# Kernel optimization log

Hardware: AMD Instinct MI355X
Metric: run time of the kernel (lower is better)

The kernel has to match this reference:

```python
import jax, jax.numpy as jnp
import numpy as np

N = 10000      # nodes
ND = 64        # node_dim
H = 128        # hidden_dim
L = 4          # num_layers
K = 16         # knn k
TD = 16        # time_dim


def _time_embed(t, n):
    # sinusoidal embedding, matches _time_embed: freqs = exp(linspace(0,1,half)*-4)
    half = TD // 2
    freqs = jnp.exp(jnp.linspace(0.0, 1.0, half) * -4.0)            # [half]
    angles = t.reshape(1, 1) * freqs[None, :]                        # [1, half]
    emb = jnp.concatenate([jnp.sin(angles), jnp.cos(angles)], -1)    # [1, TD]
    return jnp.broadcast_to(emb, (n, TD))


def _knn_edges(pos, k):
    # full cdist + topk, mirroring _knn_graph (no_grad in torch)
    n = pos.shape[0]
    sq = jnp.sum(pos * pos, -1)
    d2 = sq[:, None] + sq[None, :] - 2.0 * (pos @ pos.T)             # [N, N]
    idxr = jnp.arange(n)
    d2 = d2.at[idxr, idxr].set(jnp.inf)
    _, nbr = jax.lax.top_k(-d2, k)                                   # [N, K] nearest
    src = jnp.repeat(idxr, k)
    dst = nbr.reshape(-1)
    return src, dst


def _egnn_layer(h, pos, src, dst, s, ew1, eb1, ew2, eb2, nw1, nb1, nw2, nb2, cw, cb):
    n = h.shape[0]
    diff = pos[dst] - pos[src]                                       # [E, 3]
    r2 = jnp.sum(diff * diff, -1, keepdims=True)                     # [E, 1]
    r = jnp.sqrt(r2 + 1e-8)
    dir_ij = diff / r
    e_in = jnp.concatenate([h[dst], h[src], r2], -1)                 # [E, 2H+1]
    m = jax.nn.silu(e_in @ ew1 + eb1)
    m = jax.nn.silu(m @ ew2 + eb2)                                   # [E, H]
    m = m * s[src][:, None]                                          # s-gate
    m_sum = jax.ops.segment_sum(m, dst, num_segments=n)              # [N, H]
    deg = jax.ops.segment_sum(jnp.ones((m.shape[0], 1), m.dtype), dst, num_segments=n)
    deg = jnp.maximum(deg, 1.0)
    m_sum = m_sum / deg
    hn = jax.nn.silu(jnp.concatenate([h, m_sum], -1) @ nw1 + nb1)
    h_new = hn @ nw2 + nb2                                           # [N, H]
    gamma = m @ cw + cb                                              # [E, 1]
    cu = jax.ops.segment_sum(gamma * dir_ij, dst, num_segments=n) / deg
    return h_new, pos + cu


def setup_inputs() -> dict:
    key = jax.random.key(0)
    ks = jax.random.split(key, 24)
    g = lambda k, shape: (jax.random.normal(k, shape, dtype=jnp.float32) * 0.05)
    z = lambda shape: jnp.zeros(shape, jnp.float32)
    return {
        'x': jax.random.normal(ks[0], (N, ND), jnp.float32),
        'pos': jax.random.normal(ks[1], (N, 3), jnp.float32) * 5.0,
        't': jax.random.uniform(ks[2], (1,), jnp.float32),
        's': jax.random.uniform(ks[3], (N,), jnp.float32),
        'proj_w': g(ks[4], (ND + 1 + TD, H)), 'proj_b': z((H,)),
        'edge_w1': g(ks[5], (L, 2 * H + 1, H)), 'edge_b1': z((L, H)),
        'edge_w2': g(ks[6], (L, H, H)), 'edge_b2': z((L, H)),
        'node_w1': g(ks[7], (L, 2 * H, H)), 'node_b1': z((L, H)),
        'node_w2': g(ks[8], (L, H, H)), 'node_b2': z((L, H)),
        'coord_w': g(ks[9], (L, H, 1)), 'coord_b': z((L, 1)),
        'ec_w': g(ks[10], (H, 3)), 'ec_b': z((3,)),
        'ef_w': g(ks[11], (H, ND)), 'ef_b': z((ND,)),
    }


def reference(x, pos, t, s, proj_w, proj_b, edge_w1, edge_b1, edge_w2, edge_b2,
              node_w1, node_b1, node_w2, node_b2, coord_w, coord_b,
              ec_w, ec_b, ef_w, ef_b):
    n = x.shape[0]
    src, dst = _knn_edges(jax.lax.stop_gradient(pos), K)  # graph build is no_grad
    temb = _time_embed(t[0], n)
    h = jnp.concatenate([x, s[:, None], temb], -1) @ proj_w + proj_b  # [N, H]
    p = pos
    for l in range(L):
        h, p = _egnn_layer(h, p, src, dst, s,
                           edge_w1[l], edge_b1[l], edge_w2[l], edge_b2[l],
                           node_w1[l], node_b1[l], node_w2[l], node_b2[l],
                           coord_w[l], coord_b[l])
    eps_c = h @ ec_w + ec_b                                           # [N, 3]
    eps_f = h @ ef_w + ef_b                                           # [N, ND]
    return jnp.concatenate([eps_c, eps_f, p], -1)                     # [N, 3+ND+3]
```

## Files before the change

### kernel.cpp

```cpp
#include <hip/hip_runtime.h>
#include <math.h>

#define N_NODES 10000
#define ND 64
#define H 128
#define LAYERS 4
#define KNN 16
#define TD 16
#define E_EDGES (N_NODES * KNN)
#define KC 1250
#define TILE_E 128

typedef __attribute__((ext_vector_type(8))) short short8;
typedef __attribute__((ext_vector_type(4))) float f32x4;

__device__ __forceinline__ float silu(float x) {
  return x * __builtin_amdgcn_rcpf(1.0f + __expf(-x));
}

__device__ __forceinline__ unsigned short f2bf(float f) {
  unsigned int u = __float_as_uint(f);
  u += 0x7fffu + ((u >> 16) & 1u);
  return (unsigned short)(u >> 16);
}
__device__ __forceinline__ float bf2f(unsigned short h) {
  return __uint_as_float(((unsigned int)h) << 16);
}

__global__ __launch_bounds__(256) void pos4_kernel(const float* __restrict__ pos,
                                                   float4* __restrict__ pos4,
                                                   float* __restrict__ p0,
                                                   int* __restrict__ degi) {
  int i = blockIdx.x * 256 + threadIdx.x;
  if (i >= N_NODES) return;
  float x = pos[i * 3 + 0], y = pos[i * 3 + 1], z = pos[i * 3 + 2];
  pos4[i] = make_float4(x, y, z, x * x + y * y + z * z);
  p0[i * 3 + 0] = x;
  p0[i * 3 + 1] = y;
  p0[i * 3 + 2] = z;
  degi[i] = 0;
}

__global__ __launch_bounds__(256) void wcvt_kernel(
    const float* __restrict__ ew2, const float* __restrict__ nw1,
    const float* __restrict__ nw2, const float* __restrict__ ew1,
    const float* __restrict__ pw, const float* __restrict__ ecw,
    const float* __restrict__ efw, unsigned short* __restrict__ w2T,
    unsigned short* __restrict__ nw1T, unsigned short* __restrict__ nw2T,
    unsigned short* __restrict__ ew1T, unsigned short* __restrict__ pwT,
    unsigned short* __restrict__ owT) {
  int i = blockIdx.x * 256 + threadIdx.x;
  if (i < 65536) {
    int l = i >> 14, rem = i & 16383, c = rem >> 7, o = rem & 127;
    w2T[l * 16384 + o * 128 + c] = f2bf(ew2[i]);
  } else if (i < 196608) {
    int j = i - 65536;
    int l = j >> 15, rem = j & 32767, c2 = rem >> 7, o = rem & 127;
    nw1T[l * 32768 + o * 256 + c2] = f2bf(nw1[j]);
  } else if (i < 262144) {
    int j = i - 196608;
    int l = j >> 14, rem = j & 16383, c = rem >> 7, o = rem & 127;
    nw2T[l * 16384 + o * 128 + c] = f2bf(nw2[j]);
  } else if (i < 393216) {
    int j = i - 262144;
    int l = j >> 15, rem = j & 32767, r = rem >> 7, o = rem & 127;
    int o2 = o + ((r >> 7) << 7);
    int c = r & 127;
    ew1T[l * 32768 + o2 * 128 + c] = f2bf(ew1[l * 257 * 128 + r * 128 + o]);
  } else if (i < 405504) {
    int j = i - 393216;
    int o = j / 96, c = j - o * 96;
    pwT[j] = (c < 81) ? f2bf(pw[c * 128 + o]) : 0;
  } else {
    int j = i - 405504;
    int o = j >> 7, c = j & 127;
    float v = 0.0f;
    if (o < 3) v = ecw[c * 3 + o];
    else if (o < 67) v = efw[c * 64 + (o - 3)];
    owT[j] = f2bf(v);
  }
}

#define DIST2(pp, d0, d1)                                                    \
  d0 = fmaf(ax0, (pp).x, fmaf(ay0, (pp).y, fmaf(az0, (pp).z, (pp).w)));      \
  d1 = fmaf(ax1, (pp).x, fmaf(ay1, (pp).y, fmaf(az1, (pp).z, (pp).w)));

#define PAIR(dv0, dv1, gbase)                                                \
  {                                                                          \
    unsigned long long m0 = __ballot((dv0) < th0);                           \
    unsigned long long m1 = __ballot((dv1) < th1);                           \
    if (m0 | m1) {                                                           \
      while (m0 | m1) {                                                      \
        if (m0) {                                                            \
          int sl = __ffsll((long long)m0) - 1;                               \
          m0 &= m0 - 1;                                                      \
          float db = __shfl((dv0), sl, 64);                                  \
          int gj = (gbase) + sl;                                             \
          float pv = __shfl_up(v0, 1, 64);                                   \
          int pid = __shfl_up(id0, 1, 64);                                   \
          bool stay = (v0 <= db);                                            \
          bool tk = (lane == 0) || (pv <= db);                               \
          v0 = stay ? v0 : (tk ? db : pv);                                   \
          id0 = stay ? id0 : (tk ? gj : pid);                                \
        }                                                                    \
        if (m1) {                                                            \
          int sl = __ffsll((long long)m1) - 1;                               \
          m1 &= m1 - 1;                                                      \
          float db = __shfl((dv1), sl, 64);                                  \
          int gj = (gbase) + sl;                                             \
          float pv = __shfl_up(v1, 1, 64);                                   \
          int pid = __shfl_up(id1, 1, 64);                                   \
          bool stay = (v1 <= db);                                            \
          bool tk = (lane == 0) || (pv <= db);                               \
          v1 = stay ? v1 : (tk ? db : pv);                                   \
          id1 = stay ? id1 : (tk ? gj : pid);                                \
        }                                                                    \
      }                                                                      \
      th0 = __shfl(v0, 16, 64);                                              \
      th1 = __shfl(v1, 16, 64);                                              \
    }                                                                        \
  }

__global__ __launch_bounds__(256) void knn_kernel(const float4* __restrict__ pos4,
                                                  int* __restrict__ nbr,
                                                  int* __restrict__ degi) {
  __shared__ float4 C[KC];
  int tid = threadIdx.x;
  int lane = tid & 63;
  int wid = tid >> 6;
  int qb = blockIdx.x * 8 + wid * 2;
  float4 q0 = pos4[qb];
  float4 q1 = pos4[qb + 1];
  float ax0 = -2.0f * q0.x, ay0 = -2.0f * q0.y, az0 = -2.0f * q0.z;
  float ax1 = -2.0f * q1.x, ay1 = -2.0f * q1.y, az1 = -2.0f * q1.z;
  float v0 = __builtin_inff(), v1 = __builtin_inff();
  int id0 = 0, id1 = 0;
  float th0 = __builtin_inff(), th1 = __builtin_inff();
  for (int base = 0; base < N_NODES; base += KC) {
    __syncthreads();
    for (int jj = tid; jj < KC; jj += 256) C[jj] = pos4[base + jj];
    __syncthreads();
    for (int j0 = 0; j0 < 1024; j0 += 256) {
      float4 pA = C[j0 + lane], pB = C[j0 + 64 + lane];
      float4 pC = C[j0 + 128 + lane], pD = C[j0 + 192 + lane];
      float dA0, dA1, dB0, dB1, dC0, dC1, dD0, dD1;
      DIST2(pA, dA0, dA1);
      DIST2(pB, dB0, dB1);
      DIST2(pC, dC0, dC1);
      DIST2(pD, dD0, dD1);
      float mn0 = fminf(fminf(dA0, dB0), fminf(dC0, dD0));
      float mn1 = fminf(fminf(dA1, dB1), fminf(dC1, dD1));
      if (__ballot((mn0 < th0) | (mn1 < th1))) {
        int gb = base + j0;
        PAIR(dA0, dA1, gb);
        PAIR(dB0, dB1, gb + 64);
        PAIR(dC0, dC1, gb + 128);
        PAIR(dD0, dD1, gb + 192);
      }
    }
    {
      float4 pA = C[1024 + lane], pB = C[1088 + lane], pC = C[1152 + lane];
      float dA0, dA1, dB0, dB1, dC0, dC1;
      float dD0 = __builtin_inff(), dD1 = __builtin_inff();
      DIST2(pA, dA0, dA1);
      DIST2(pB, dB0, dB1);
      DIST2(pC, dC0, dC1);
      if (lane < 34) {
        float4 pD = C[1216 + lane];
        DIST2(pD, dD0, dD1);
      }
      float mn0 = fminf(fminf(dA0, dB0), fminf(dC0, dD0));
      float mn1 = fminf(fminf(dA1, dB1), fminf(dC1, dD1));
      if (__ballot((mn0 < th0) | (mn1 < th1))) {
        int gb = base + 1024;
        PAIR(dA0, dA1, gb);
        PAIR(dB0, dB1, gb + 64);
        PAIR(dC0, dC1, gb + 128);
        PAIR(dD0, dD1, gb + 192);
      }
    }
  }
  if (lane >= 1 && lane < 17) {
    nbr[qb * KNN + lane - 1] = id0;
    atomicAdd(&degi[id0], 1);
    nbr[(qb + 1) * KNN + lane - 1] = id1;
    atomicAdd(&degi[id1], 1);
  }
}

__global__ __launch_bounds__(1024) void scan_kernel(const int* __restrict__ degi,
                                                    int* __restrict__ off,
                                                    int* __restrict__ cursor) {
  __shared__ int part[1024];
  int t = threadIdx.x;
  int base = t * 10;
  int sum = 0;
  if (t < 1000)
    for (int i = 0; i < 10; ++i) sum += degi[base + i];
  part[t] = sum;
  __syncthreads();
  for (int stp = 1; stp < 1024; stp <<= 1) {
    int v = (t >= stp) ? part[t - stp] : 0;
    __syncthreads();
    part[t] += v;
    __syncthreads();
  }
  if (t < 1000) {
    int run = (t == 0) ? 0 : part[t - 1];
    for (int i = 0; i < 10; ++i) {
      off[base + i] = run;
      cursor[base + i] = run;
      run += degi[base + i];
    }
  }
  if (t == 0) off[N_NODES] = E_EDGES;
}

__global__ void scatter_kernel(const int* __restrict__ nbr, int* __restrict__ cursor,
                               int* __restrict__ eid, int* __restrict__ dstof) {
  int e = blockIdx.x * 256 + threadIdx.x;
  if (e < E_EDGES) {
    int d = nbr[e];
    int p = atomicAdd(&cursor[d], 1);
    eid[p] = e;
    dstof[p] = d;
  }
}

__global__ void sort_kernel(const int* __restrict__ off, int* __restrict__ eid) {
  int n = blockIdx.x * 256 + threadIdx.x;
  if (n >= N_NODES) return;
  int a = off[n], b = off[n + 1];
  for (int i = a + 1; i < b; ++i) {
    int v = eid[i];
    int j = i - 1;
    while (j >= a && eid[j] > v) { eid[j + 1] = eid[j]; --j; }
    eid[j + 1] = v;
  }
}

__global__ __launch_bounds__(256) void proj_ab_kernel(
    const float* __restrict__ x, const float* __restrict__ s,
    const float* __restrict__ tptr, const unsigned short* __restrict__ pwT,
    const float* __restrict__ pb, const unsigned short* __restrict__ ew1T,
    const float* __restrict__ eb1, float* __restrict__ h_out,
    unsigned short* __restrict__ Abf, unsigned short* __restrict__ Bbf) {
  __shared__ unsigned short inpb[16][104];
  __shared__ unsigned short hb[16][136];
  int tid = threadIdx.x;
  int n0 = blockIdx.x * 16;
  float t = tptr[0];
  for (int idx = tid; idx < 16 * 104; idx += 256) {
    int n = idx / 104, c = idx - n * 104;
    int gn = n0 + n;
    float val;
    if (c < 64) val = x[gn * ND + c];
    else if (c == 64) val = s[gn];
    else if (c < 81) {
      int j = c - 65;
      int jj = (j < 8) ? j : (j - 8);
      float f = __expf(-4.0f * (float)jj / 7.0f);
      float a = t * f;
      val = (j < 8) ? sinf(a) : cosf(a);
    } else val = 0.0f;
    inpb[n][c] = f2bf(val);
  }
  __syncthreads();
  int w = tid >> 6, lane = tid & 63, fr = lane & 15, kg = lane >> 4;
  f32x4 acc[2];
  acc[0] = (f32x4){0.f, 0.f, 0.f, 0.f};
  acc[1] = (f32x4){0.f, 0.f, 0.f, 0.f};
#pragma unroll
  for (int ks = 0; ks < 3; ++ks) {
    int k = ks * 32 + kg * 8;
    short8 a = *(const short8*)&inpb[fr][k];
#pragma unroll
    for (int nt = 0; nt < 2; ++nt) {
      int col = w * 32 + nt * 16 + fr;
      short8 b = *(const short8*)&pwT[col * 96 + k];
      acc[nt] = __builtin_amdgcn_mfma_f32_16x16x32_bf16(a, b, acc[nt], 0, 0, 0);
    }
  }
#pragma unroll
  for (int nt = 0; nt < 2; ++nt) {
    int col = w * 32 + nt * 16 + fr;
    float bias = pb[col];
#pragma unroll
    for (int r = 0; r < 4; ++r) {
      int row = kg * 4 + r;
      float hv = acc[nt][r] + bias;
      h_out[(n0 + row) * H + col] = hv;
      hb[row][col] = f2bf(hv);
    }
  }
  __syncthreads();
  f32x4 acc2[4];
#pragma unroll
  for (int nt = 0; nt < 4; ++nt) acc2[nt] = (f32x4){0.f, 0.f, 0.f, 0.f};
#pragma unroll
  for (int ks = 0; ks < 4; ++ks) {
    int k = ks * 32 + kg * 8;
    short8 a = *(const short8*)&hb[fr][k];
#pragma unroll
    for (int nt = 0; nt < 4; ++nt) {
      int col = w * 64 + nt * 16 + fr;
      short8 b = *(const short8*)&ew1T[col * H + k];
      acc2[nt] = __builtin_amdgcn_mfma_f32_16x16x32_bf16(a, b, acc2[nt], 0, 0, 0);
    }
  }
#pragma unroll
  for (int nt = 0; nt < 4; ++nt) {
    int col = w * 64 + nt * 16 + fr;
    float bias = (col < H) ? eb1[col] : 0.0f;
#pragma unroll
    for (int r = 0; r < 4; ++r) {
      int row = kg * 4 + r;
      float val = acc2[nt][r] + bias;
      if (col < H) Abf[(n0 + row) * H + col] = f2bf(val);
      else Bbf[(n0 + row) * H + (col - H)] = f2bf(val);
    }
  }
}

__global__ __launch_bounds__(256) void edge_mfma_kernel(
    const unsigned short* __restrict__ Abf, const unsigned short* __restrict__ Bbf,
    const float* __restrict__ p, const float* __restrict__ s,
    const int* __restrict__ csr_off, const int* __restrict__ eid,
    const int* __restrict__ dstof, const float* __restrict__ wr,
    const unsigned short* __restrict__ w2T, const float* __restrict__ eb2,
    const float* __restrict__ cw, const float* __restrict__ cbp,
    float* __restrict__ msA, float* __restrict__ msB,
    float* __restrict__ cuA, float* __restrict__ cuB) {
  __shared__ unsigned short t1s[TILE_E][136];
  __shared__ float r2A[TILE_E], sA[TILE_E], dirA[TILE_E][3], gA[TILE_E];
  __shared__ float gpart[2][TILE_E];
  __shared__ int srcA[TILE_E], dstA[TILE_E];
  __shared__ float wrs[H], b2s[H], cws[H];

  int tid = threadIdx.x;
  int P0 = blockIdx.x * TILE_E;
  int P1 = P0 + TILE_E;

  if (tid < H) { wrs[tid] = wr[tid]; b2s[tid] = eb2[tid]; cws[tid] = cw[tid]; }
  if (tid < TILE_E) {
    int e = tid;
    int edge = eid[P0 + e];
    int src = edge >> 4;
    int d = dstof[P0 + e];
    srcA[e] = src;
    dstA[e] = d;
    float dx = p[d * 3 + 0] - p[src * 3 + 0];
    float dy = p[d * 3 + 1] - p[src * 3 + 1];
    float dz = p[d * 3 + 2] - p[src * 3 + 2];
    float r2 = dx * dx + dy * dy + dz * dz;
    r2A[e] = r2;
    float rinv = 1.0f / sqrtf(r2 + 1e-8f);
    dirA[e][0] = dx * rinv;
    dirA[e][1] = dy * rinv;
    dirA[e][2] = dz * rinv;
    sA[e] = s[src];
  }
  __syncthreads();

  int nA = dstA[0], nB = dstA[TILE_E - 1];
  int nn = nB - nA + 1;

  for (int idx = tid; idx < TILE_E * 16; idx += 256) {
    int e = idx >> 4, cp = (idx & 15) * 8;
    uint4 au = *(const uint4*)&Abf[dstA[e] * H + cp];
    uint4 bu = *(const uint4*)&Bbf[srcA[e] * H + cp];
    float r2v = r2A[e];
    unsigned int as[4] = {au.x, au.y, au.z, au.w};
    unsigned int bs[4] = {bu.x, bu.y, bu.z, bu.w};
    unsigned int res[4];
#pragma unroll
    for (int q = 0; q < 4; ++q) {
      float pr0 = silu(bf2f((unsigned short)(as[q] & 0xffffu)) +
                       bf2f((unsigned short)(bs[q] & 0xffffu)) +
                       r2v * wrs[cp + 2 * q]);
      float pr1 = silu(bf2f((unsigned short)(as[q] >> 16)) +
                       bf2f((unsigned short)(bs[q] >> 16)) +
                       r2v * wrs[cp + 2 * q + 1]);
      res[q] = ((unsigned int)f2bf(pr1) << 16) | (unsigned int)f2bf(pr0);
    }
    *(uint4*)&t1s[e][cp] = make_uint4(res[0], res[1], res[2], res[3]);
  }
  __syncthreads();

  int w = tid >> 6, lane = tid & 63;
  int fr = lane & 15, kg = lane >> 4;
  f32x4 acc[8][2];
#pragma unroll
  for (int mt = 0; mt < 8; ++mt)
#pragma unroll
    for (int nt = 0; nt < 2; ++nt) acc[mt][nt] = (f32x4){0.f, 0.f, 0.f, 0.f};
#pragma unroll
  for (int ks = 0; ks < 4; ++ks) {
    int k = ks * 32 + kg * 8;
    short8 bf0 = *(const short8*)&w2T[(w * 32 + fr) * H + k];
    short8 bf1 = *(const short8*)&w2T[(w * 32 + 16 + fr) * H + k];
#pragma unroll
    for (int mt = 0; mt < 8; ++mt) {
      short8 a = *(const short8*)&t1s[mt * 16 + fr][k];
      acc[mt][0] = __builtin_amdgcn_mfma_f32_16x16x32_bf16(a, bf0, acc[mt][0], 0, 0, 0);
      acc[mt][1] = __builtin_amdgcn_mfma_f32_16x16x32_bf16(a, bf1, acc[mt][1], 0, 0, 0);
    }
  }
  __syncthreads();

#pragma unroll
  for (int mt = 0; mt < 8; ++mt) {
#pragma unroll
    for (int nt = 0; nt < 2; ++nt) {
      int col = w * 32 + nt * 16 + fr;
      float b2v = b2s[col];
#pragma unroll
      for (int r = 0; r < 4; ++r) {
        int row = mt * 16 + kg * 4 + r;
        float mv = silu(acc[mt][nt][r] + b2v) * sA[row];
        t1s[row][col] = f2bf(mv);
      }
    }
  }
  __syncthreads();

  {
    int e = tid & 127, half = tid >> 7;
    int c0 = half * 64;
    float g = 0.f;
    for (int c = c0; c < c0 + 64; c += 4) {
      uint2 u = *(const uint2*)&t1s[e][c];
      g = fmaf(bf2f((unsigned short)(u.x & 0xffffu)), cws[c], g);
      g = fmaf(bf2f((unsigned short)(u.x >> 16)), cws[c + 1], g);
      g = fmaf(bf2f((unsigned short)(u.y & 0xffffu)), cws[c + 2], g);
      g = fmaf(bf2f((unsigned short)(u.y >> 16)), cws[c + 3], g);
    }
    gpart[half][e] = g;
  }
  __syncthreads();
  if (tid < TILE_E) gA[tid] = gpart[0][tid] + gpart[1][tid] + cbp[0];
  __syncthreads();

  for (int idx = tid; idx < nn * 32; idx += 256) {
    int ni = idx >> 5, cq = (idx & 31) * 4;
    int n = nA + ni;
    int o0 = csr_off[n], o1 = csr_off[n + 1];
    int lo = max(o0, P0), hi = min(o1, P1);
    float s0 = 0.f, s1 = 0.f, s2 = 0.f, s3 = 0.f;
    for (int pos = lo; pos < hi; ++pos) {
      uint2 u = *(const uint2*)&t1s[pos - P0][cq];
      s0 += bf2f((unsigned short)(u.x & 0xffffu));
      s1 += bf2f((unsigned short)(u.x >> 16));
      s2 += bf2f((unsigned short)(u.y & 0xffffu));
      s3 += bf2f((unsigned short)(u.y >> 16));
    }
    float4 sv = make_float4(s0, s1, s2, s3);
    if (o0 >= P0) {
      *(float4*)&msA[n * H + cq] = sv;
      if (o1 <= P1) *(float4*)&msB[n * H + cq] = make_float4(0.f, 0.f, 0.f, 0.f);
    } else {
      *(float4*)&msB[n * H + cq] = sv;
    }
  }
  for (int idx = tid; idx < nn * 3; idx += 256) {
    int ni = idx / 3, comp = idx - ni * 3;
    int n = nA + ni;
    int o0 = csr_off[n], o1 = csr_off[n + 1];
    int lo = max(o0, P0), hi = min(o1, P1);
    float sum = 0.f;
    for (int pos = lo; pos < hi; ++pos)
      sum += gA[pos - P0] * dirA[pos - P0][comp];
    if (o0 >= P0) {
      cuA[n * 3 + comp] = sum;
      if (o1 <= P1) cuB[n * 3 + comp] = 0.0f;
    } else {
      cuB[n * 3 + comp] = sum;
    }
  }
}

__global__ __launch_bounds__(256) void node_mfma_kernel(
    const float* __restrict__ h, const float* __restrict__ msA,
    const float* __restrict__ msB, const int* __restrict__ degi,
    const float* __restrict__ cuA, const float* __restrict__ cuB,
    const float* __restrict__ p_in, const unsigned short* __restrict__ w1T,
    const float* __restrict__ nb1, const unsigned short* __restrict__ w2T,
    const float* __restrict__ nb2, const unsigned short* __restrict__ ew1Tn,
    const float* __restrict__ eb1n, int doab, float* __restrict__ h_out,
    float* __restrict__ p_out, unsigned short* __restrict__ Abf,
    unsigned short* __restrict__ Bbf) {
  __shared__ unsigned short insb[16][264];
  __shared__ unsigned short hnsb[16][136];
  int tid = threadIdx.x;
  int n0 = blockIdx.x * 16;
  for (int idx = tid; idx < 16 * 32; idx += 256) {
    int n = idx >> 5, cq = (idx & 31) * 4;
    int gn = n0 + n;
    float4 hv = *(const float4*)&h[gn * H + cq];
    int dg = degi[gn];
    float m0 = 0.f, m1 = 0.f, m2 = 0.f, m3 = 0.f;
    if (dg > 0) {
      float4 a = *(const float4*)&msA[gn * H + cq];
      float4 b = *(const float4*)&msB[gn * H + cq];
      float fdg = (float)dg;
      m0 = (a.x + b.x) / fdg;
      m1 = (a.y + b.y) / fdg;
      m2 = (a.z + b.z) / fdg;
      m3 = (a.w + b.w) / fdg;
    }
    uint2 uh, um;
    uh.x = ((unsigned int)f2bf(hv.y) << 16) | (unsigned int)f2bf(hv.x);
    uh.y = ((unsigned int)f2bf(hv.w) << 16) | (unsigned int)f2bf(hv.z);
    um.x = ((unsigned int)f2bf(m1) << 16) | (unsigned int)f2bf(m0);
    um.y = ((unsigned int)f2bf(m3) << 16) | (unsigned int)f2bf(m2);
    *(uint2*)&insb[n][cq] = uh;
    *(uint2*)&insb[n][H + cq] = um;
  }
  __syncthreads();
  int w = tid >> 6, lane = tid & 63, fr = lane & 15, kg = lane >> 4;
  f32x4 acc[2];
  acc[0] = (f32x4){0.f, 0.f, 0.f, 0.f};
  acc[1] = (f32x4){0.f, 0.f, 0.f, 0.f};
#pragma unroll
  for (int ks = 0; ks < 8; ++ks) {
    int k = ks * 32 + kg * 8;
    short8 a = *(const short8*)&insb[fr][k];
#pragma unroll
    for (int nt = 0; nt < 2; ++nt) {
      int col = w * 32 + nt * 16 + fr;
      short8 b = *(const short8*)&w1T[col * 256 + k];
      acc[nt] = __builtin_amdgcn_mfma_f32_16x16x32_bf16(a, b, acc[nt], 0, 0, 0);
    }
  }
#pragma unroll
  for (int nt = 0; nt < 2; ++nt) {
    int col = w * 32 + nt * 16 + fr;
    float b1 = nb1[col];
#pragma unroll
    for (int r = 0; r < 4; ++r) {
      int row = kg * 4 + r;
      hnsb[row][col] = f2bf(silu(acc[nt][r] + b1));
    }
  }
  __syncthreads();
  f32x4 acc2[2];
  acc2[0] = (f32x4){0.f, 0.f, 0.f, 0.f};
  acc2[1] = (f32x4){0.f, 0.f, 0.f, 0.f};
#pragma unroll
  for (int ks = 0; ks < 4; ++ks) {
    int k = ks * 32 + kg * 8;
    short8 a = *(const short8*)&hnsb[fr][k];
#pragma unroll
    for (int nt = 0; nt < 2; ++nt) {
      int col = w * 32 + nt * 16 + fr;
      short8 b = *(const short8*)&w2T[col * H + k];
      acc2[nt] = __builtin_amdgcn_mfma_f32_16x16x32_bf16(a, b, acc2[nt], 0, 0, 0);
    }
  }
  unsigned short (*hb)[136] = (unsigned short(*)[136])insb;
#pragma unroll
  for (int nt = 0; nt < 2; ++nt) {
    int col = w * 32 + nt * 16 + fr;
    float b2 = nb2[col];
#pragma unroll
    for (int r = 0; r < 4; ++r) {
      int row = kg * 4 + r;
      float hv = acc2[nt][r] + b2;
      h_out[(n0 + row) * H + col] = hv;
      hb[row][col] = f2bf(hv);
    }
  }
  if (tid < 48) {
    int nl = tid / 3, comp = tid - nl * 3;
    int gn = n0 + nl;
    int dg = degi[gn];
    float add = 0.0f;
    if (dg > 0)
      add = (cuA[gn * 3 + comp] + cuB[gn * 3 + comp]) / (float)dg;
    p_out[gn * 3 + comp] = p_in[gn * 3 + comp] + add;
  }
  if (doab) {
    __syncthreads();
    f32x4 acc3[4];
#pragma unroll
    for (int nt = 0; nt < 4; ++nt) acc3[nt] = (f32x4){0.f, 0.f, 0.f, 0.f};
#pragma unroll
    for (int ks = 0; ks < 4; ++ks) {
      int k = ks * 32 + kg * 8;
      short8 a = *(const short8*)&hb[fr][k];
#pragma unroll
      for (int nt = 0; nt < 4; ++nt) {
        int col = w * 64 + nt * 16 + fr;
        short8 b = *(const short8*)&ew1Tn[col * H + k];
        acc3[nt] = __builtin_amdgcn_mfma_f32_16x16x32_bf16(a, b, acc3[nt], 0, 0, 0);
      }
    }
#pragma unroll
    for (int nt = 0; nt < 4; ++nt) {
      int col = w * 64 + nt * 16 + fr;
      float bias = (col < H) ? eb1n[col] : 0.0f;
#pragma unroll
      for (int r = 0; r < 4; ++r) {
        int row = kg * 4 + r;
        float val = acc3[nt][r] + bias;
        if (col < H) Abf[(n0 + row) * H + col] = f2bf(val);
        else Bbf[(n0 + row) * H + (col - H)] = f2bf(val);
      }
    }
  }
}

__global__ __launch_bounds__(256) void out_mfma_kernel(
    const float* __restrict__ h, const float* __restrict__ p,
    const unsigned short* __restrict__ owT, const float* __restrict__ ecb,
    const float* __restrict__ efb, float* __restrict__ out) {
  __shared__ unsigned short hb[16][136];
  int tid = threadIdx.x;
  int n0 = blockIdx.x * 16;
  for (int idx = tid; idx < 16 * H; idx += 256) {
    int n = idx >> 7, c = idx & 127;
    hb[n][c] = f2bf(h[(n0 + n) * H + c]);
  }
  __syncthreads();
  int w = tid >> 6, lane = tid & 63, fr = lane & 15, kg = lane >> 4;
  int ntiles = (w == 0) ? 2 : 1;
  for (int tt = 0; tt < ntiles; ++tt) {
    int tile = (tt == 0) ? w : 4;
    f32x4 acc = (f32x4){0.f, 0.f, 0.f, 0.f};
    int col = tile * 16 + fr;
#pragma unroll
    for (int ks = 0; ks < 4; ++ks) {
      int k = ks * 32 + kg * 8;
      short8 a = *(const short8*)&hb[fr][k];
      short8 b = *(const short8*)&owT[col * H + k];
      acc = __builtin_amdgcn_mfma_f32_16x16x32_bf16(a, b, acc, 0, 0, 0);
    }
    if (col < 67) {
      float bias = (col < 3) ? ecb[col] : efb[col - 3];
#pragma unroll
      for (int r = 0; r < 4; ++r) {
        int row = kg * 4 + r;
        out[(n0 + row) * 70 + col] = acc[r] + bias;
      }
    }
  }
  if (tid < 48) {
    int nl = tid / 3, comp = tid - nl * 3;
    int gn = n0 + nl;
    out[gn * 70 + 67 + comp] = p[gn * 3 + comp];
  }
}

extern "C" void kernel_launch(void* const* d_in, const int* in_sizes, int n_in,
                              void* d_out, int out_size, void* d_ws, size_t ws_size,
                              hipStream_t stream) {
  const float* x = (const float*)d_in[0];
  const float* pos = (const float*)d_in[1];
  const float* t = (const float*)d_in[2];
  const float* s = (const float*)d_in[3];
  const float* pw = (const float*)d_in[4];
  const float* pb = (const float*)d_in[5];
  const float* ew1 = (const float*)d_in[6];
  const float* eb1 = (const float*)d_in[7];
  const float* ew2 = (const float*)d_in[8];
  const float* eb2 = (const float*)d_in[9];
  const float* nw1 = (const float*)d_in[10];
  const float* nb1 = (const float*)d_in[11];
  const float* nw2 = (const float*)d_in[12];
  const float* nb2 = (const float*)d_in[13];
  const float* cw = (const float*)d_in[14];
  const float* cb = (const float*)d_in[15];
  const float* ecw = (const float*)d_in[16];
  const float* ecb = (const float*)d_in[17];
  const float* efw = (const float*)d_in[18];
  const float* efb = (const float*)d_in[19];

  char* wp = (char*)d_ws;
  auto alloc = [&](size_t bytes) {
    char* r = wp;
    wp += (bytes + 255) & ~(size_t)255;
    return r;
  };
  float* h0 = (float*)alloc((size_t)N_NODES * H * 4);
  float* h1 = (float*)alloc((size_t)N_NODES * H * 4);
  unsigned short* Abf = (unsigned short*)alloc((size_t)N_NODES * H * 2);
  unsigned short* Bbf = (unsigned short*)alloc((size_t)N_NODES * H * 2);
  float* msAb = (float*)alloc((size_t)N_NODES * H * 4);
  float* msBb = (float*)alloc((size_t)N_NODES * H * 4);
  float* cuAb = (float*)alloc((size_t)N_NODES * 3 * 4);
  float* cuBb = (float*)alloc((size_t)N_NODES * 3 * 4);
  float* p0 = (float*)alloc((size_t)N_NODES * 3 * 4);
  float* p1 = (float*)alloc((size_t)N_NODES * 3 * 4);
  int* degi = (int*)alloc((size_t)N_NODES * 4);
  int* nbr = (int*)alloc((size_t)E_EDGES * 4);
  int* off = (int*)alloc((size_t)(N_NODES + 1) * 4);
  int* cursor = (int*)alloc((size_t)N_NODES * 4);
  int* eid = (int*)alloc((size_t)E_EDGES * 4);
  int* dstof = (int*)alloc((size_t)E_EDGES * 4);
  unsigned short* w2Tb = (unsigned short*)alloc((size_t)LAYERS * H * H * 2);
  unsigned short* nw1Tb = (unsigned short*)alloc((size_t)LAYERS * 2 * H * H * 2);
  unsigned short* nw2Tb = (unsigned short*)alloc((size_t)LAYERS * H * H * 2);
  unsigned short* ew1Tb = (unsigned short*)alloc((size_t)LAYERS * 2 * H * H * 2);
  unsigned short* pwTb = (unsigned short*)alloc((size_t)H * 96 * 2);
  unsigned short* owTb = (unsigned short*)alloc((size_t)80 * H * 2);

  float4* pos4 = (float4*)msAb;

  wcvt_kernel<<<1624, 256, 0, stream>>>(ew2, nw1, nw2, ew1, pw, ecw, efw,
                                        w2Tb, nw1Tb, nw2Tb, ew1Tb, pwTb, owTb);
  pos4_kernel<<<(N_NODES + 255) / 256, 256, 0, stream>>>(pos, pos4, p0, degi);
  knn_kernel<<<N_NODES / 8, 256, 0, stream>>>(pos4, nbr, degi);
  scan_kernel<<<1, 1024, 0, stream>>>(degi, off, cursor);
  scatter_kernel<<<(E_EDGES + 255) / 256, 256, 0, stream>>>(nbr, cursor, eid, dstof);
  sort_kernel<<<(N_NODES + 255) / 256, 256, 0, stream>>>(off, eid);
  proj_ab_kernel<<<N_NODES / 16, 256, 0, stream>>>(x, s, t, pwTb, pb, ew1Tb, eb1,
                                                   h0, Abf, Bbf);

  float* hc = h0;
  float* hn = h1;
  float* pc = p0;
  float* pn = p1;
  for (int l = 0; l < LAYERS; ++l) {
    const float* ew1l = ew1 + (size_t)l * 257 * H;
    int doab = (l < LAYERS - 1) ? 1 : 0;
    edge_mfma_kernel<<<E_EDGES / TILE_E, 256, 0, stream>>>(
        Abf, Bbf, pc, s, off, eid, dstof, ew1l + 256 * H,
        w2Tb + (size_t)l * H * H, eb2 + l * H, cw + l * H, cb + l,
        msAb, msBb, cuAb, cuBb);
    node_mfma_kernel<<<N_NODES / 16, 256, 0, stream>>>(
        hc, msAb, msBb, degi, cuAb, cuBb, pc, nw1Tb + (size_t)l * 2 * H * H,
        nb1 + l * H, nw2Tb + (size_t)l * H * H, nb2 + l * H,
        ew1Tb + (size_t)(l + doab) * 2 * H * H, eb1 + (size_t)(l + doab) * H,
        doab, hn, pn, Abf, Bbf);
    float* tmp = hc; hc = hn; hn = tmp;
    tmp = pc; pc = pn; pn = tmp;
  }
  out_mfma_kernel<<<N_NODES / 16, 256, 0, stream>>>(hc, pc, owTb, ecb, efb,
                                                    (float*)d_out);
}
```

Measured before the change: 401.0 us.

## Fuse setup kernels, mask self in KNN, use DPP/readlane for insertion

Merges the weight-conversion and position-prep kernels into one launch, and merges the per-node edge sort into the projection kernel, so the chain has fewer launches and fewer dependent gaps. In the KNN kernel the self-distance is now masked to infinity, which drops the extra self slot so only the top 16 are kept and the threshold is read from lane 15. The insertion-sort shuffles are replaced with DPP row shifts and readlane. The DPP shift with row mask 0xF moves values only within 16-lane rows, which is enough here because the kept list lives in lanes 0-15, but it adds per-tile compare work for the self mask.

Result: faster. 369.5 us (-7.8%).

```diff
diff --git a/kernel.cpp b/kernel.cpp
--- a/kernel.cpp
+++ b/kernel.cpp
@@ -10,6 +10,7 @@
 #define E_EDGES (N_NODES * KNN)
 #define KC 1250
 #define TILE_E 128
+#define INF __builtin_inff()
 
 typedef __attribute__((ext_vector_type(8))) short short8;
 typedef __attribute__((ext_vector_type(4))) float f32x4;
@@ -27,63 +28,88 @@
   return __uint_as_float(((unsigned int)h) << 16);
 }
 
-__global__ __launch_bounds__(256) void pos4_kernel(const float* __restrict__ pos,
-                                                   float4* __restrict__ pos4,
-                                                   float* __restrict__ p0,
-                                                   int* __restrict__ degi) {
-  int i = blockIdx.x * 256 + threadIdx.x;
-  if (i >= N_NODES) return;
-  float x = pos[i * 3 + 0], y = pos[i * 3 + 1], z = pos[i * 3 + 2];
-  pos4[i] = make_float4(x, y, z, x * x + y * y + z * z);
-  p0[i * 3 + 0] = x;
-  p0[i * 3 + 1] = y;
-  p0[i * 3 + 2] = z;
-  degi[i] = 0;
-}
-
-__global__ __launch_bounds__(256) void wcvt_kernel(
+__device__ __forceinline__ float dpp_shr1_f(float x) {
+  return __int_as_float(__builtin_amdgcn_update_dpp(
+      0, __float_as_int(x), 0x111, 0xF, 0xF, true));
+}
+__device__ __forceinline__ int dpp_shr1_i(int x) {
+  return __builtin_amdgcn_update_dpp(0, x, 0x111, 0xF, 0xF, true);
+}
+__device__ __forceinline__ float rdlane_f(float x, int sl) {
+  return __int_as_float(__builtin_amdgcn_readlane(__float_as_int(x), sl));
+}
+
+__global__ __launch_bounds__(256) void init_kernel(
     const float* __restrict__ ew2, const float* __restrict__ nw1,
     const float* __restrict__ nw2, const float* __restrict__ ew1,
     const float* __restrict__ pw, const float* __restrict__ ecw,
     const float* __restrict__ efw, unsigned short* __restrict__ w2T,
     unsigned short* __restrict__ nw1T, unsigned short* __restrict__ nw2T,
     unsigned short* __restrict__ ew1T, unsigned short* __restrict__ pwT,
-    unsigned short* __restrict__ owT) {
-  int i = blockIdx.x * 256 + threadIdx.x;
-  if (i < 65536) {
-    int l = i >> 14, rem = i & 16383, c = rem >> 7, o = rem & 127;
-    w2T[l * 16384 + o * 128 + c] = f2bf(ew2[i]);
-  } else if (i < 196608) {
-    int j = i - 65536;
-    int l = j >> 15, rem = j & 32767, c2 = rem >> 7, o = rem & 127;
-    nw1T[l * 32768 + o * 256 + c2] = f2bf(nw1[j]);
-  } else if (i < 262144) {
-    int j = i - 196608;
-    int l = j >> 14, rem = j & 16383, c = rem >> 7, o = rem & 127;
-    nw2T[l * 16384 + o * 128 + c] = f2bf(nw2[j]);
-  } else if (i < 393216) {
-    int j = i - 262144;
-    int l = j >> 15, rem = j & 32767, r = rem >> 7, o = rem & 127;
-    int o2 = o + ((r >> 7) << 7);
-    int c = r & 127;
-    ew1T[l * 32768 + o2 * 128 + c] = f2bf(ew1[l * 257 * 128 + r * 128 + o]);
-  } else if (i < 405504) {
-    int j = i - 393216;
-    int o = j / 96, c = j - o * 96;
-    pwT[j] = (c < 81) ? f2bf(pw[c * 128 + o]) : 0;
+    unsigned short* __restrict__ owT, const float* __restrict__ pos,
+    float4* __restrict__ pos4, float* __restrict__ p0,
+    int* __restrict__ degi) {
+  int bid = blockIdx.x;
+  if (bid < 1624) {
+    int i = bid * 256 + threadIdx.x;
+    if (i < 65536) {
+      int l = i >> 14, rem = i & 16383, c = rem >> 7, o = rem & 127;
+      w2T[l * 16384 + o * 128 + c] = f2bf(ew2[i]);
+    } else if (i < 196608) {
+      int j = i - 65536;
+      int l = j >> 15, rem = j & 32767, c2 = rem >> 7, o = rem & 127;
+      nw1T[l * 32768 + o * 256 + c2] = f2bf(nw1[j]);
+    } else if (i < 262144) {
+      int j = i - 196608;
+      int l = j >> 14, rem = j & 16383, c = rem >> 7, o = rem & 127;
+      nw2T[l * 16384 + o * 128 + c] = f2bf(nw2[j]);
+    } else if (i < 393216) {
+      int j = i - 262144;
+      int l = j >> 15, rem = j & 32767, r = rem >> 7, o = rem & 127;
+      int o2 = o + ((r >> 7) << 7);
+      int c = r & 127;
+      ew1T[l * 32768 + o2 * 128 + c] = f2bf(ew1[l * 257 * 128 + r * 128 + o]);
+    } else if (i < 405504) {
+      int j = i - 393216;
+      int o = j / 96, c = j - o * 96;
+      pwT[j] = (c < 81) ? f2bf(pw[c * 128 + o]) : 0;
+    } else if (i < 415744) {
+      int j = i - 405504;
+      int o = j >> 7, c = j & 127;
+      float v = 0.0f;
+      if (o < 3) v = ecw[c * 3 + o];
+      else if (o < 67) v = efw[c * 64 + (o - 3)];
+      owT[j] = f2bf(v);
+    }
   } else {
-    int j = i - 405504;
-    int o = j >> 7, c = j & 127;
-    float v = 0.0f;
-    if (o < 3) v = ecw[c * 3 + o];
-    else if (o < 67) v = efw[c * 64 + (o - 3)];
-    owT[j] = f2bf(v);
+    int i = (bid - 1624) * 256 + threadIdx.x;
+    if (i >= N_NODES) return;
+    float x = pos[i * 3 + 0], y = pos[i * 3 + 1], z = pos[i * 3 + 2];
+    pos4[i] = make_float4(x, y, z, x * x + y * y + z * z);
+    p0[i * 3 + 0] = x;
+    p0[i * 3 + 1] = y;
+    p0[i * 3 + 2] = z;
+    degi[i] = 0;
   }
 }
 
 #define DIST2(pp, d0, d1)                                                    \
   d0 = fmaf(ax0, (pp).x, fmaf(ay0, (pp).y, fmaf(az0, (pp).z, (pp).w)));      \
   d1 = fmaf(ax1, (pp).x, fmaf(ay1, (pp).y, fmaf(az1, (pp).z, (pp).w)));
+
+#define INS1(dv, V, ID, gbase, mreg)                                         \
+  if (mreg) {                                                                \
+    int sl = __ffsll((long long)mreg) - 1;                                   \
+    mreg &= mreg - 1;                                                        \
+    float db = rdlane_f((dv), sl);                                           \
+    int gj = (gbase) + sl;                                                   \
+    float pv = dpp_shr1_f(V);                                                \
+    int pid = dpp_shr1_i(ID);                                                \
+    bool stay = ((V) <= db);                                                 \
+    bool tk = (lane == 0) || (pv <= db);                                     \
+    (V) = stay ? (V) : (tk ? db : pv);                                       \
+    (ID) = stay ? (ID) : (tk ? gj : pid);                                    \
+  }
 
 #define PAIR(dv0, dv1, gbase)                                                \
   {                                                                          \
@@ -91,33 +117,11 @@
     unsigned long long m1 = __ballot((dv1) < th1);                           \
     if (m0 | m1) {                                                           \
       while (m0 | m1) {                                                      \
-        if (m0) {                                                            \
-          int sl = __ffsll((long long)m0) - 1;                               \
-          m0 &= m0 - 1;                                                      \
-          float db = __shfl((dv0), sl, 64);                                  \
-          int gj = (gbase) + sl;                                             \
-          float pv = __shfl_up(v0, 1, 64);                                   \
-          int pid = __shfl_up(id0, 1, 64);                                   \
-          bool stay = (v0 <= db);                                            \
-          bool tk = (lane == 0) || (pv <= db);                               \
-          v0 = stay ? v0 : (tk ? db : pv);                                   \
-          id0 = stay ? id0 : (tk ? gj : pid);                                \
-        }                                                                    \
-        if (m1) {                                                            \
-          int sl = __ffsll((long long)m1) - 1;                               \
-          m1 &= m1 - 1;                                                      \
-          float db = __shfl((dv1), sl, 64);                                  \
-          int gj = (gbase) + sl;                                             \
-          float pv = __shfl_up(v1, 1, 64);                                   \
-          int pid = __shfl_up(id1, 1, 64);                                   \
-          bool stay = (v1 <= db);                                            \
-          bool tk = (lane == 0) || (pv <= db);                               \
-          v1 = stay ? v1 : (tk ? db : pv);                                   \
-          id1 = stay ? id1 : (tk ? gj : pid);                                \
-        }                                                                    \
+        INS1(dv0, v0, id0, gbase, m0);                                       \
+        INS1(dv1, v1, id1, gbase, m1);                                       \
       }                                                                      \
-      th0 = __shfl(v0, 16, 64);                                              \
-      th1 = __shfl(v1, 16, 64);                                              \
+      th0 = rdlane_f(v0, 15);                                                \
+      th1 = rdlane_f(v1, 15);                                                \
     }                                                                        \
   }
 
@@ -133,9 +137,9 @@
   float4 q1 = pos4[qb + 1];
   float ax0 = -2.0f * q0.x, ay0 = -2.0f * q0.y, az0 = -2.0f * q0.z;
   float ax1 = -2.0f * q1.x, ay1 = -2.0f * q1.y, az1 = -2.0f * q1.z;
-  float v0 = __builtin_inff(), v1 = __builtin_inff();
+  float v0 = INF, v1 = INF;
   int id0 = 0, id1 = 0;
-  float th0 = __builtin_inff(), th1 = __builtin_inff();
+  float th0 = INF, th1 = INF;
   for (int base = 0; base < N_NODES; base += KC) {
     __syncthreads();
     for (int jj = tid; jj < KC; jj += 256) C[jj] = pos4[base + jj];
@@ -148,6 +152,15 @@
       DIST2(pB, dB0, dB1);
       DIST2(pC, dC0, dC1);
       DIST2(pD, dD0, dD1);
+      int ga = base + j0 + lane;
+      if (ga == qb) dA0 = INF;
+      if (ga == qb + 1) dA1 = INF;
+      if (ga + 64 == qb) dB0 = INF;
+      if (ga + 64 == qb + 1) dB1 = INF;
+      if (ga + 128 == qb) dC0 = INF;
+      if (ga + 128 == qb + 1) dC1 = INF;
+      if (ga + 192 == qb) dD0 = INF;
+      if (ga + 192 == qb + 1) dD1 = INF;
       float mn0 = fminf(fminf(dA0, dB0), fminf(dC0, dD0));
       float mn1 = fminf(fminf(dA1, dB1), fminf(dC1, dD1));
       if (__ballot((mn0 < th0) | (mn1 < th1))) {
@@ -161,7 +174,7 @@
     {
       float4 pA = C[1024 + lane], pB = C[1088 + lane], pC = C[1152 + lane];
       float dA0, dA1, dB0, dB1, dC0, dC1;
-      float dD0 = __builtin_inff(), dD1 = __builtin_inff();
+      float dD0 = INF, dD1 = INF;
       DIST2(pA, dA0, dA1);
       DIST2(pB, dB0, dB1);
       DIST2(pC, dC0, dC1);
@@ -169,6 +182,15 @@
         float4 pD = C[1216 + lane];
         DIST2(pD, dD0, dD1);
       }
+      int ga = base + 1024 + lane;
+      if (ga == qb) dA0 = INF;
+      if (ga == qb + 1) dA1 = INF;
+      if (ga + 64 == qb) dB0 = INF;
+      if (ga + 64 == qb + 1) dB1 = INF;
+      if (ga + 128 == qb) dC0 = INF;
+      if (ga + 128 == qb + 1) dC1 = INF;
+      if (ga + 192 == qb) dD0 = INF;
+      if (ga + 192 == qb + 1) dD1 = INF;
       float mn0 = fminf(fminf(dA0, dB0), fminf(dC0, dD0));
       float mn1 = fminf(fminf(dA1, dB1), fminf(dC1, dD1));
       if (__ballot((mn0 < th0) | (mn1 < th1))) {
@@ -180,10 +202,10 @@
       }
     }
   }
-  if (lane >= 1 && lane < 17) {
-    nbr[qb * KNN + lane - 1] = id0;
+  if (lane < KNN) {
+    nbr[qb * KNN + lane] = id0;
     atomicAdd(&degi[id0], 1);
-    nbr[(qb + 1) * KNN + lane - 1] = id1;
+    nbr[(qb + 1) * KNN + lane] = id1;
     atomicAdd(&degi[id1], 1);
   }
 }
@@ -227,28 +249,30 @@
   }
 }
 
-__global__ void sort_kernel(const int* __restrict__ off, int* __restrict__ eid) {
-  int n = blockIdx.x * 256 + threadIdx.x;
-  if (n >= N_NODES) return;
-  int a = off[n], b = off[n + 1];
-  for (int i = a + 1; i < b; ++i) {
-    int v = eid[i];
-    int j = i - 1;
-    while (j >= a && eid[j] > v) { eid[j + 1] = eid[j]; --j; }
-    eid[j + 1] = v;
-  }
-}
-
-__global__ __launch_bounds__(256) void proj_ab_kernel(
+__global__ __launch_bounds__(256) void sort_proj_kernel(
     const float* __restrict__ x, const float* __restrict__ s,
     const float* __restrict__ tptr, const unsigned short* __restrict__ pwT,
     const float* __restrict__ pb, const unsigned short* __restrict__ ew1T,
     const float* __restrict__ eb1, float* __restrict__ h_out,
-    unsigned short* __restrict__ Abf, unsigned short* __restrict__ Bbf) {
+    unsigned short* __restrict__ Abf, unsigned short* __restrict__ Bbf,
+    const int* __restrict__ off, int* __restrict__ eid) {
   __shared__ unsigned short inpb[16][104];
   __shared__ unsigned short hb[16][136];
   int tid = threadIdx.x;
-  int n0 = blockIdx.x * 16;
+  int bid = blockIdx.x;
+  if (bid >= 625) {
+    int n = (bid - 625) * 256 + tid;
+    if (n >= N_NODES) return;
+    int a = off[n], b = off[n + 1];
+    for (int i = a + 1; i < b; ++i) {
+      int v = eid[i];
+      int j = i - 1;
+      while (j >= a && eid[j] > v) { eid[j + 1] = eid[j]; --j; }
+      eid[j + 1] = v;
+    }
+    return;
+  }
+  int n0 = bid * 16;
   float t = tptr[0];
   for (int idx = tid; idx < 16 * 104; idx += 256) {
     int n = idx / 104, c = idx - n * 104;
@@ -706,15 +730,14 @@
 
   float4* pos4 = (float4*)msAb;
 
-  wcvt_kernel<<<1624, 256, 0, stream>>>(ew2, nw1, nw2, ew1, pw, ecw, efw,
-                                        w2Tb, nw1Tb, nw2Tb, ew1Tb, pwTb, owTb);
-  pos4_kernel<<<(N_NODES + 255) / 256, 256, 0, stream>>>(pos, pos4, p0, degi);
+  init_kernel<<<1664, 256, 0, stream>>>(ew2, nw1, nw2, ew1, pw, ecw, efw,
+                                        w2Tb, nw1Tb, nw2Tb, ew1Tb, pwTb, owTb,
+                                        pos, pos4, p0, degi);
   knn_kernel<<<N_NODES / 8, 256, 0, stream>>>(pos4, nbr, degi);
   scan_kernel<<<1, 1024, 0, stream>>>(degi, off, cursor);
   scatter_kernel<<<(E_EDGES + 255) / 256, 256, 0, stream>>>(nbr, cursor, eid, dstof);
-  sort_kernel<<<(N_NODES + 255) / 256, 256, 0, stream>>>(off, eid);
-  proj_ab_kernel<<<N_NODES / 16, 256, 0, stream>>>(x, s, t, pwTb, pb, ew1Tb, eb1,
-                                                   h0, Abf, Bbf);
+  sort_proj_kernel<<<665, 256, 0, stream>>>(x, s, t, pwTb, pb, ew1Tb, eb1,
+                                            h0, Abf, Bbf, off, eid);
 
   float* hc = h0;
   float* hn = h1;
```
